# Optimization experiments

Hardware: AMD Instinct MI355X
Metric: run time of the kernel (lower is better)

The kernel has to match this reference:

```python
import jax, jax.numpy as jnp
import numpy as np


def _feature_map(x):
    # elu_feature_map: F.elu(x) + 1
    return jax.nn.elu(x) + 1.0


def setup_inputs() -> dict:
    key = jax.random.key(0)
    kq, kk, kv = jax.random.split(key, 3)
    B, H, S, D = 4, 16, 2048, 64
    Q = jax.random.normal(kq, (B, H, S, D), dtype=jnp.float32)
    K = jax.random.normal(kk, (B, H, S, D), dtype=jnp.float32)
    V = jax.random.normal(kv, (B, H, S, D), dtype=jnp.float32)
    return {"Q": Q, "K": K, "V": V}


def reference(Q, K, V):
    Qf = _feature_map(Q)  # [B,H,S,D]
    Kf = _feature_map(K)  # [B,H,S,D]
    scores = jnp.einsum('bhsd,bhtd->bhst', Qf, Kf)  # [B,H,S,S]
    attn = jax.nn.softmax(scores, axis=-1)
    out = jnp.einsum('bhst,bhtd->bhsd', attn, V)  # [B,H,S,D]
    return out
```

## Files before the change

### kernel.cpp

```cpp
#include <hip/hip_runtime.h>
#include <stdint.h>

typedef __attribute__((ext_vector_type(8))) _Float16 f16x8;
typedef __attribute__((ext_vector_type(2))) _Float16 f16x2;
typedef __attribute__((ext_vector_type(8))) short bf16x8;
typedef __attribute__((ext_vector_type(16))) float f32x16;

#define BH_ 64
#define S_ 2048
#define D_ 64
#define KT_ 64
#define NT_ (S_ / KT_)
#define LOG2E 1.44269504088896340736f
#define DEFER_THR 14.0f

#define WS_ARR ((size_t)BH_ * S_ * D_ * 2)
#define WS_NEED (2 * WS_ARR)

__device__ __forceinline__ uint16_t f32_to_bf16_rn(float f) {
    uint32_t u = __float_as_uint(f);
    u += 0x7fffu + ((u >> 16) & 1u);
    return (uint16_t)(u >> 16);
}
__device__ __forceinline__ float bfbits_to_f32(uint16_t h) {
    return __uint_as_float(((uint32_t)h) << 16);
}
__device__ __forceinline__ float phi(float x) { return x > 0.0f ? x + 1.0f : __expf(x); }

#if __has_builtin(__builtin_amdgcn_exp2f)
#define EXP2F(x) __builtin_amdgcn_exp2f(x)
#else
#define EXP2F(x) exp2f(x)
#endif

__device__ __forceinline__ float fmax3(float a, float b, float c) {
    float d;
    asm("v_max3_f32 %0, %1, %2, %3" : "=v"(d) : "v"(a), "v"(b), "v"(c));
    return d;
}

__device__ __forceinline__ uint32_t pkrtz(float lo, float hi2) {
    union {
        decltype(__builtin_amdgcn_cvt_pkrtz(0.0f, 0.0f)) v;
        uint32_t u;
    } c;
    c.v = __builtin_amdgcn_cvt_pkrtz(lo, hi2);
    return c.u;
}

__device__ __forceinline__ float dot2acc(uint32_t p2, float acc) {
#if __has_builtin(__builtin_amdgcn_fdot2)
    union { uint32_t u; f16x2 v; } c;
    c.u = p2;
    const f16x2 one2 = {(_Float16)1.0f, (_Float16)1.0f};
    return __builtin_amdgcn_fdot2(c.v, one2, acc, false);
#else
    union { uint32_t u; f16x2 v; } c;
    c.u = p2;
    return acc + (float)c.v[0] + (float)c.v[1];
#endif
}

#define GLL16(gsrc, ldst)                                                              \
    __builtin_amdgcn_global_load_lds(                                                  \
        (const __attribute__((address_space(1))) uint32_t*)(gsrc),                     \
        (__attribute__((address_space(3))) uint32_t*)(ldst), 16, 0, 0)


__global__ void prep_k(const float* __restrict__ K, uint16_t* __restrict__ Kf) {
    const size_t e = ((size_t)blockIdx.x * 256 + threadIdx.x) * 8;
    const int d0 = (int)(e & 63);
    const int c = d0 >> 3;
    const int t = (int)((e >> 6) & 63);
    const size_t dst = e - d0 + (size_t)((c ^ (t & 7) ^ ((t >> 3) & 7)) * 8);
    const float4 a = *(const float4*)(K + e);
    const float4 b = *(const float4*)(K + e + 4);
    const float xs[8] = {a.x, a.y, a.z, a.w, b.x, b.y, b.z, b.w};
    _Float16 h8[8];
#pragma unroll
    for (int j = 0; j < 8; ++j) h8[j] = (_Float16)phi(xs[j]);
    *(f16x8*)(Kf + dst) = *(const f16x8*)h8;
}

__global__ void prep_v(const float* __restrict__ V, uint16_t* __restrict__ Vt) {
    const int bh = blockIdx.x >> 5, kt = blockIdx.x & 31;
    const int d = threadIdx.x >> 2;
    const size_t tile = (size_t)(bh * 32 + kt) * 4096;
    const float* vb = V + ((size_t)bh * S_ + (size_t)kt * KT_) * D_ + d;
#pragma unroll
    for (int cc = 0; cc < 2; ++cc) {
        const int ct = (threadIdx.x & 3) * 2 + cc;
        _Float16 v8[8];
#pragma unroll
        for (int i = 0; i < 8; ++i) {
            const int pos = 8 * ct + i;
            const int src = (pos & 48) | (4 * ((pos >> 3) & 1) + (pos & 3) + 8 * ((pos >> 2) & 1));
            v8[i] = (_Float16)vb[(size_t)src * D_];
        }
        *(f16x8*)(Vt + tile + (size_t)d * 64 +
                  (size_t)((ct ^ (d & 7) ^ ((d >> 3) & 7)) * 8)) = *(const f16x8*)v8;
    }
}


__global__ __launch_bounds__(512, 4)
void la_attn8(const float* __restrict__ Q, const uint16_t* __restrict__ Kf,
              const uint16_t* __restrict__ Vt, float* __restrict__ O)
{
    const int id = blockIdx.x;
    const int wg = (id & 7) * 64 + (id >> 3);
    const int bh = wg >> 3;
    const int qt = wg & 7;
    const int tid = threadIdx.x;
    const int lane = tid & 63;
    const int wid = tid >> 6;
    const int ln31 = lane & 31;
    const int hi = lane >> 5;
    const int sw = (ln31 & 7) ^ (ln31 >> 3);

    __shared__ __align__(16) uint16_t kf_s[2][4096];
    __shared__ __align__(16) uint16_t vt_s[2][4096];

    const int q0 = qt * 256 + wid * 32;

    f16x8 qf[4];
    {
        const float* qp = Q + ((size_t)bh * S_ + q0 + ln31) * 64;
#pragma unroll
        for (int m = 0; m < 4; ++m) {
            const float4 a = *(const float4*)(qp + m * 16 + hi * 8);
            const float4 b = *(const float4*)(qp + m * 16 + hi * 8 + 4);
            const float xs[8] = {a.x, a.y, a.z, a.w, b.x, b.y, b.z, b.w};
            _Float16 h8[8];
#pragma unroll
            for (int j = 0; j < 8; ++j) h8[j] = (_Float16)(phi(xs[j]) * LOG2E);
            qf[m] = *(const f16x8*)h8;
        }
    }

    int off4[4];
#pragma unroll
    for (int m = 0; m < 4; ++m)
        off4[m] = ln31 * 64 + (((2 * m + hi) ^ sw) * 8);

    f32x16 accO0 = (f32x16)0.0f, accO1 = (f32x16)0.0f;
    float m_run = 0.0f, l_run = 0.0f;

    const size_t tb0 = (size_t)bh * 32 * 4096;

    auto stage = [&](int buf, int kt2) {
        const size_t toff = tb0 + (size_t)kt2 * 4096 + (size_t)tid * 8;
        GLL16(Kf + toff, &kf_s[buf][tid * 8]);
        GLL16(Vt + toff, &vt_s[buf][tid * 8]);
    };

    stage(0, 0);
    int cur = 0;

    for (int kt = 0; kt < NT_; ++kt) {
        __syncthreads();
        if (kt + 1 < NT_) stage(cur ^ 1, kt + 1);

        const uint16_t* __restrict__ kfp = kf_s[cur];
        const uint16_t* __restrict__ vtp = vt_s[cur];

        f32x16 s0, s1;
#pragma unroll
        for (int r = 0; r < 16; ++r) { s0[r] = -m_run; s1[r] = -m_run; }
        __builtin_amdgcn_s_setprio(1);
#pragma unroll
        for (int m = 0; m < 4; ++m) {
            f16x8 k0 = *(const f16x8*)&kfp[off4[m]];
            f16x8 k1 = *(const f16x8*)&kfp[(off4[m] ^ 32) + 2048];
            s0 = __builtin_amdgcn_mfma_f32_32x32x16_f16(k0, qf[m], s0, 0, 0, 0);
            s1 = __builtin_amdgcn_mfma_f32_32x32x16_f16(k1, qf[m], s1, 0, 0, 0);
        }
        __builtin_amdgcn_s_setprio(0);

        float t8[8];
#pragma unroll
        for (int r = 0; r < 8; ++r)
            t8[r] = fmax3(fmaxf(s0[r], s0[r + 8]), s1[r], s1[r + 8]);
        const float ta = fmax3(t8[0], t8[1], t8[2]);
        const float tb = fmax3(t8[3], t8[4], t8[5]);
        const float tc = fmaxf(t8[6], t8[7]);
        float tmax = fmax3(ta, tb, tc);
        tmax = fmaxf(tmax, __shfl_xor(tmax, 32));

        if (!__all(tmax <= DEFER_THR)) {
            const float dlt = fmaxf(tmax, 0.0f);
            const float corr = EXP2F(-dlt);
            m_run += dlt;
            l_run *= corr;
#pragma unroll
            for (int r = 0; r < 16; ++r) {
                accO0[r] *= corr; accO1[r] *= corr;
                s0[r] -= dlt; s1[r] -= dlt;
            }
        }
#pragma unroll
        for (int r = 0; r < 16; ++r) {
            s0[r] = EXP2F(s0[r]);
            s1[r] = EXP2F(s1[r]);
        }

        union PF { uint32_t u[4]; f16x8 v; };
        PF pf[4];
#pragma unroll
        for (int i = 0; i < 4; ++i) {
            pf[0].u[i] = pkrtz(s0[2 * i], s0[2 * i + 1]);
            pf[1].u[i] = pkrtz(s0[8 + 2 * i], s0[9 + 2 * i]);
            pf[2].u[i] = pkrtz(s1[2 * i], s1[2 * i + 1]);
            pf[3].u[i] = pkrtz(s1[8 + 2 * i], s1[9 + 2 * i]);
        }

        float lsA = 0.0f, lsB = 0.0f;
#pragma unroll
        for (int i = 0; i < 4; ++i) {
            lsA = dot2acc(pf[0].u[i], lsA);
            lsB = dot2acc(pf[1].u[i], lsB);
            lsA = dot2acc(pf[2].u[i], lsA);
            lsB = dot2acc(pf[3].u[i], lsB);
        }
        l_run += lsA + lsB;

        __builtin_amdgcn_s_setprio(1);
#pragma unroll
        for (int c = 0; c < 4; ++c) {
            f16x8 v0 = *(const f16x8*)&vtp[off4[c]];
            f16x8 v1 = *(const f16x8*)&vtp[(off4[c] ^ 32) + 2048];
            accO0 = __builtin_amdgcn_mfma_f32_32x32x16_f16(v0, pf[c].v, accO0, 0, 0, 0);
            accO1 = __builtin_amdgcn_mfma_f32_32x32x16_f16(v1, pf[c].v, accO1, 0, 0, 0);
        }
        __builtin_amdgcn_s_setprio(0);

        cur ^= 1;
    }

    const float l_tot = l_run + __shfl_xor(l_run, 32);
    const float inv = 1.0f / l_tot;
    float* op = O + ((size_t)bh * S_ + q0 + ln31) * D_;
#pragma unroll
    for (int g = 0; g < 4; ++g) {
        float4 o0, o1;
        o0.x = accO0[4 * g + 0] * inv; o0.y = accO0[4 * g + 1] * inv;
        o0.z = accO0[4 * g + 2] * inv; o0.w = accO0[4 * g + 3] * inv;
        o1.x = accO1[4 * g + 0] * inv; o1.y = accO1[4 * g + 1] * inv;
        o1.z = accO1[4 * g + 2] * inv; o1.w = accO1[4 * g + 3] * inv;
        *(float4*)(op + 8 * g + 4 * hi) = o0;
        *(float4*)(op + 32 + 8 * g + 4 * hi) = o1;
    }
}


__global__ __launch_bounds__(256, 2)
void la_attn_fwd(const float* __restrict__ Q, const float* __restrict__ K,
                 const float* __restrict__ V, float* __restrict__ O)
{
    const int bh = blockIdx.x;
    const int qt = blockIdx.y;
    const int tid = threadIdx.x;
    const int lane = tid & 63;
    const int wid = tid >> 6;
    const int ln31 = lane & 31;
    const int hi = lane >> 5;

    const size_t base = (size_t)bh * (S_ * D_);
    const float* __restrict__ Qb = Q + base;
    const float* __restrict__ Kb = K + base;
    const float* __restrict__ Vb = V + base;
    float* __restrict__ Ob = O + base;

    __shared__ __align__(16) uint16_t kh[32][D_];
    __shared__ __align__(16) uint16_t kl[32][D_];

    const int q0 = qt * 128 + wid * 32;

    bf16x8 qfh[4], qfl[4];
    {
        const float* qp = Qb + (size_t)(q0 + ln31) * D_;
#pragma unroll
        for (int m = 0; m < 4; ++m) {
            const float4 a = *(const float4*)(qp + m * 16 + hi * 8);
            const float4 b = *(const float4*)(qp + m * 16 + hi * 8 + 4);
            float xs[8] = {a.x, a.y, a.z, a.w, b.x, b.y, b.z, b.w};
#pragma unroll
            for (int j = 0; j < 8; ++j) {
                float x = phi(xs[j]);
                uint16_t h = f32_to_bf16_rn(x);
                qfh[m][j] = (short)h;
                qfl[m][j] = (short)f32_to_bf16_rn(x - bfbits_to_f32(h));
            }
        }
    }

    f32x16 accO0 = (f32x16)0.0f;
    f32x16 accO1 = (f32x16)0.0f;
    float m_run = -1e30f;
    float l_run = 0.0f;

    const int srow = tid >> 3;
    const int scolu = (tid & 7) << 3;
    const int scsw = scolu ^ ((srow & 7) << 3);

    for (int kt = 0; kt < S_ / 32; ++kt) {
        const int tb = kt * 32;
        {
            const float* kp = Kb + (size_t)(tb + srow) * D_ + scolu;
            const float4 a = *(const float4*)(kp);
            const float4 b = *(const float4*)(kp + 4);
            float xs[8] = {a.x, a.y, a.z, a.w, b.x, b.y, b.z, b.w};
            short h8[8], l8[8];
#pragma unroll
            for (int j = 0; j < 8; ++j) {
                float x = phi(xs[j]);
                uint16_t h = f32_to_bf16_rn(x);
                h8[j] = (short)h;
                l8[j] = (short)f32_to_bf16_rn(x - bfbits_to_f32(h));
            }
            *(bf16x8*)&kh[srow][scsw] = *(const bf16x8*)h8;
            *(bf16x8*)&kl[srow][scsw] = *(const bf16x8*)l8;
        }
        __syncthreads();

        f32x16 accS = (f32x16)0.0f;
#pragma unroll
        for (int m = 0; m < 4; ++m) {
            const int c = (m * 16 + hi * 8) ^ ((ln31 & 7) << 3);
            bf16x8 kfh = *(const bf16x8*)&kh[ln31][c];
            bf16x8 kfl = *(const bf16x8*)&kl[ln31][c];
            accS = __builtin_amdgcn_mfma_f32_32x32x16_bf16(kfh, qfh[m], accS, 0, 0, 0);
            accS = __builtin_amdgcn_mfma_f32_32x32x16_bf16(kfh, qfl[m], accS, 0, 0, 0);
            accS = __builtin_amdgcn_mfma_f32_32x32x16_bf16(kfl, qfh[m], accS, 0, 0, 0);
        }

        float tmax = accS[0];
#pragma unroll
        for (int r = 1; r < 16; ++r) tmax = fmaxf(tmax, accS[r]);
        tmax = fmaxf(tmax, __shfl_xor(tmax, 32));
        const float m_new = fmaxf(m_run, tmax);
        const float corr = __expf(m_run - m_new);
        m_run = m_new;

        float p[16];
        float psum = 0.0f;
#pragma unroll
        for (int r = 0; r < 16; ++r) { p[r] = __expf(accS[r] - m_new); psum += p[r]; }
        l_run = l_run * corr + psum;

#pragma unroll
        for (int r = 0; r < 16; ++r) { accO0[r] *= corr; accO1[r] *= corr; }

        uint32_t pk[8];
#pragma unroll
        for (int k2 = 0; k2 < 8; ++k2)
            pk[k2] = (uint32_t)f32_to_bf16_rn(p[2 * k2]) |
                     ((uint32_t)f32_to_bf16_rn(p[2 * k2 + 1]) << 16);

        const uint32_t s0 = hi ? pk[0] : pk[2];
        const uint32_t s1 = hi ? pk[1] : pk[3];
        const uint32_t s2 = hi ? pk[4] : pk[6];
        const uint32_t s3 = hi ? pk[5] : pk[7];
        const uint32_t r0 = __shfl_xor(s0, 32);
        const uint32_t r1 = __shfl_xor(s1, 32);
        const uint32_t r2 = __shfl_xor(s2, 32);
        const uint32_t r3 = __shfl_xor(s3, 32);

        union U { uint32_t u[4]; bf16x8 v; };
        U f0, f1;
        f0.u[0] = hi ? r0 : pk[0];  f0.u[1] = hi ? r1 : pk[1];
        f0.u[2] = hi ? pk[2] : r0;  f0.u[3] = hi ? pk[3] : r1;
        f1.u[0] = hi ? r2 : pk[4];  f1.u[1] = hi ? r3 : pk[5];
        f1.u[2] = hi ? pk[6] : r2;  f1.u[3] = hi ? pk[7] : r3;

#pragma unroll
        for (int ts = 0; ts < 2; ++ts) {
            const bf16x8 pfv = ts ? f1.v : f0.v;
            const float* vp = Vb + (size_t)(tb + ts * 16 + hi * 8) * D_ + ln31;
#pragma unroll
            for (int dn = 0; dn < 2; ++dn) {
                bf16x8 vf;
#pragma unroll
                for (int j = 0; j < 8; ++j)
                    vf[j] = (short)f32_to_bf16_rn(vp[(size_t)j * D_ + dn * 32]);
                if (dn == 0) accO0 = __builtin_amdgcn_mfma_f32_32x32x16_bf16(vf, pfv, accO0, 0, 0, 0);
                else         accO1 = __builtin_amdgcn_mfma_f32_32x32x16_bf16(vf, pfv, accO1, 0, 0, 0);
            }
        }
        __syncthreads();
    }

    const float l_tot = l_run + __shfl_xor(l_run, 32);
    const float inv = 1.0f / l_tot;
    float* op = Ob + (size_t)(q0 + ln31) * D_;
#pragma unroll
    for (int g = 0; g < 4; ++g) {
        float4 o0, o1;
        o0.x = accO0[4 * g + 0] * inv; o0.y = accO0[4 * g + 1] * inv;
        o0.z = accO0[4 * g + 2] * inv; o0.w = accO0[4 * g + 3] * inv;
        o1.x = accO1[4 * g + 0] * inv; o1.y = accO1[4 * g + 1] * inv;
        o1.z = accO1[4 * g + 2] * inv; o1.w = accO1[4 * g + 3] * inv;
        *(float4*)(op + 8 * g + 4 * hi) = o0;
        *(float4*)(op + 32 + 8 * g + 4 * hi) = o1;
    }
}

extern "C" void kernel_launch(void* const* d_in, const int* in_sizes, int n_in,
                              void* d_out, int out_size, void* d_ws, size_t ws_size,
                              hipStream_t stream) {
    (void)in_sizes; (void)n_in; (void)out_size;
    const float* Q = (const float*)d_in[0];
    const float* K = (const float*)d_in[1];
    const float* V = (const float*)d_in[2];
    float* O = (float*)d_out;

    if (ws_size >= WS_NEED) {
        uint16_t* Kf = (uint16_t*)d_ws;
        uint16_t* Vt = (uint16_t*)((char*)d_ws + 1 * WS_ARR);
        prep_k<<<4096, 256, 0, stream>>>(K, Kf);
        prep_v<<<2048, 256, 0, stream>>>(V, Vt);
        la_attn8<<<512, 512, 0, stream>>>(Q, Kf, Vt, O);
    } else {
        la_attn_fwd<<<dim3(BH_, S_ / 128), 256, 0, stream>>>(Q, K, V, O);
    }
}
```

Measured before the change: 107.0 us.

## Software-pipeline QK^T of next tile with PV of current tile

Restructures the main loop so the score MFMAs for tile t+1 are issued alongside the PV MFMAs for tile t, with K staged two tiles ahead and V one tile ahead on separate schedules. It also moves the cross-half max shuffle into the rare rescale branch and lowers launch bounds from 4 to 2 blocks per CU to give the extra live accumulators more registers. The aim is to hide softmax/exp latency behind matrix work, at the cost of register pressure and lower occupancy.

```diff
diff --git a/kernel.cpp b/kernel.cpp
--- a/kernel.cpp
+++ b/kernel.cpp
@@ -103,7 +103,7 @@
 }
 
 
-__global__ __launch_bounds__(512, 4)
+__global__ __launch_bounds__(512, 2)
 void la_attn8(const float* __restrict__ Q, const uint16_t* __restrict__ Kf,
               const uint16_t* __restrict__ Vt, float* __restrict__ O)
 {
@@ -148,25 +148,25 @@
 
     const size_t tb0 = (size_t)bh * 32 * 4096;
 
-    auto stage = [&](int buf, int kt2) {
+    auto stageK = [&](int buf, int kt2) {
         const size_t toff = tb0 + (size_t)kt2 * 4096 + (size_t)tid * 8;
         GLL16(Kf + toff, &kf_s[buf][tid * 8]);
+    };
+    auto stageV = [&](int buf, int kt2) {
+        const size_t toff = tb0 + (size_t)kt2 * 4096 + (size_t)tid * 8;
         GLL16(Vt + toff, &vt_s[buf][tid * 8]);
     };
 
-    stage(0, 0);
-    int cur = 0;
-
-    for (int kt = 0; kt < NT_; ++kt) {
-        __syncthreads();
-        if (kt + 1 < NT_) stage(cur ^ 1, kt + 1);
-
-        const uint16_t* __restrict__ kfp = kf_s[cur];
-        const uint16_t* __restrict__ vtp = vt_s[cur];
-
-        f32x16 s0, s1;
-#pragma unroll
-        for (int r = 0; r < 16; ++r) { s0[r] = -m_run; s1[r] = -m_run; }
+    stageK(0, 0);
+    stageV(0, 0);
+    __syncthreads();
+    stageK(1, 1);
+
+    f32x16 s0, s1;
+    {
+        const uint16_t* __restrict__ kfp = kf_s[0];
+        s0 = (f32x16)0.0f;
+        s1 = (f32x16)0.0f;
         __builtin_amdgcn_s_setprio(1);
 #pragma unroll
         for (int m = 0; m < 4; ++m) {
@@ -176,6 +176,13 @@
             s1 = __builtin_amdgcn_mfma_f32_32x32x16_f16(k1, qf[m], s1, 0, 0, 0);
         }
         __builtin_amdgcn_s_setprio(0);
+    }
+
+#pragma unroll 2
+    for (int t = 0; t < NT_; ++t) {
+        __syncthreads();
+        if (t + 2 < NT_) stageK(t & 1, t + 2);
+        if (t + 1 < NT_) stageV((t + 1) & 1, t + 1);
 
         float t8[8];
 #pragma unroll
@@ -184,11 +191,10 @@
         const float ta = fmax3(t8[0], t8[1], t8[2]);
         const float tb = fmax3(t8[3], t8[4], t8[5]);
         const float tc = fmaxf(t8[6], t8[7]);
-        float tmax = fmax3(ta, tb, tc);
-        tmax = fmaxf(tmax, __shfl_xor(tmax, 32));
+        const float tmax = fmax3(ta, tb, tc);
 
         if (!__all(tmax <= DEFER_THR)) {
-            const float dlt = fmaxf(tmax, 0.0f);
+            const float dlt = fmaxf(fmaxf(tmax, __shfl_xor(tmax, 32)), 0.0f);
             const float corr = EXP2F(-dlt);
             m_run += dlt;
             l_run *= corr;
@@ -214,6 +220,33 @@
             pf[3].u[i] = pkrtz(s1[8 + 2 * i], s1[9 + 2 * i]);
         }
 
+        const bool more = (t + 1 < NT_);
+        f32x16 n0, n1;
+        __builtin_amdgcn_s_setprio(1);
+        if (more) {
+            const uint16_t* __restrict__ kfp = kf_s[(t + 1) & 1];
+            n0 = (f32x16)(-m_run);
+            n1 = (f32x16)(-m_run);
+#pragma unroll
+            for (int m = 0; m < 4; ++m) {
+                f16x8 k0 = *(const f16x8*)&kfp[off4[m]];
+                f16x8 k1 = *(const f16x8*)&kfp[(off4[m] ^ 32) + 2048];
+                n0 = __builtin_amdgcn_mfma_f32_32x32x16_f16(k0, qf[m], n0, 0, 0, 0);
+                n1 = __builtin_amdgcn_mfma_f32_32x32x16_f16(k1, qf[m], n1, 0, 0, 0);
+            }
+        }
+        {
+            const uint16_t* __restrict__ vtp = vt_s[t & 1];
+#pragma unroll
+            for (int c = 0; c < 4; ++c) {
+                f16x8 v0 = *(const f16x8*)&vtp[off4[c]];
+                f16x8 v1 = *(const f16x8*)&vtp[(off4[c] ^ 32) + 2048];
+                accO0 = __builtin_amdgcn_mfma_f32_32x32x16_f16(v0, pf[c].v, accO0, 0, 0, 0);
+                accO1 = __builtin_amdgcn_mfma_f32_32x32x16_f16(v1, pf[c].v, accO1, 0, 0, 0);
+            }
+        }
+        __builtin_amdgcn_s_setprio(0);
+
         float lsA = 0.0f, lsB = 0.0f;
 #pragma unroll
         for (int i = 0; i < 4; ++i) {
@@ -224,17 +257,7 @@
         }
         l_run += lsA + lsB;
 
-        __builtin_amdgcn_s_setprio(1);
-#pragma unroll
-        for (int c = 0; c < 4; ++c) {
-            f16x8 v0 = *(const f16x8*)&vtp[off4[c]];
-            f16x8 v1 = *(const f16x8*)&vtp[(off4[c] ^ 32) + 2048];
-            accO0 = __builtin_amdgcn_mfma_f32_32x32x16_f16(v0, pf[c].v, accO0, 0, 0, 0);
-            accO1 = __builtin_amdgcn_mfma_f32_32x32x16_f16(v1, pf[c].v, accO1, 0, 0, 0);
-        }
-        __builtin_amdgcn_s_setprio(0);
-
-        cur ^= 1;
+        if (more) { s0 = n0; s1 = n1; }
     }
 
     const float l_tot = l_run + __shfl_xor(l_run, 32);
```

Result: slower. 110.6 us (+3.3%).
